# Optimization experiments

Measured on AMD Instinct MI355X. Metric: run time of the kernel, lower is better.

## Reference

```python
import jax, jax.numpy as jnp
import numpy as np

N_NODES = 1_000_000   # G.number_of_nodes()
F = 128               # feature_size
ED = 32               # embedding_dim = 2**int(log2(F/4))
N_CAT = 1000          # int64 feature cardinality
DF = 32               # float32 feature dim
L = [524288, 131072, 32768, 8192]  # nodeflow layer sizes (0..n_layers)
FAN = 10              # sampling fanout per block
N_LAYERS = 3


def lrelu(x, slope=0.1):
    return jnp.where(x >= 0, x, slope * x)


def setup_inputs() -> dict:
    key = jax.random.key(0)
    ks = iter(jax.random.split(key, 64))
    inp = {}
    # --- nodeflow data per layer ---
    for i, Li in enumerate(L):
        inp[f"nid{i}"] = jax.random.randint(next(ks), (Li,), 0, N_NODES)
        inp[f"cat{i}"] = jax.random.randint(next(ks), (Li,), 0, N_CAT)
        inp[f"feat{i}"] = jax.random.normal(next(ks), (Li, DF), jnp.float32)
    # --- block edge lists (src in layer b, dst in layer b+1, fanout FAN) ---
    for b in range(N_LAYERS):
        E = L[b + 1] * FAN
        inp[f"src{b}"] = jax.random.randint(next(ks), (E,), 0, L[b])
        inp[f"dst{b}"] = jnp.repeat(jnp.arange(L[b + 1]), FAN)
    # --- parameters ---
    def xav(shape):
        fan_in, fan_out = shape[0], shape[-1]
        s = float(np.sqrt(6.0 / (fan_in + fan_out)))
        return jax.random.uniform(next(ks), shape, jnp.float32, -s, s)
    inp["node_emb"] = jax.random.normal(next(ks), (N_NODES + 1, ED), jnp.float32) * (1.0 / ED)
    inp["exp_W"] = xav((ED, F)); inp["exp_b"] = jax.random.normal(next(ks), (F,), jnp.float32) * 0.001
    emb_cat = jax.random.normal(next(ks), (N_CAT, F), jnp.float32) * (1.0 / F)
    inp["emb_cat"] = emb_cat.at[0].set(0.0)  # padding_idx=0
    inp["proj_W"] = xav((DF, F)); inp["proj_b"] = jax.random.normal(next(ks), (F,), jnp.float32) * 0.001
    inp["d_W1"] = xav((F, F)); inp["d_b1"] = jax.random.normal(next(ks), (F,), jnp.float32) * 0.001
    inp["d_W2"] = xav((F, F)); inp["d_b2"] = jax.random.normal(next(ks), (F,), jnp.float32) * 0.001
    # GraphSAGE convs: depth-2 MLP on [h, mean_agg] per block (stacked over blocks)
    inp["conv_W1"] = jnp.stack([xav((2 * F, F)) for _ in range(N_LAYERS)])
    inp["conv_b1"] = jax.random.normal(next(ks), (N_LAYERS, F), jnp.float32) * 0.001
    inp["conv_W2"] = jnp.stack([xav((F, F)) for _ in range(N_LAYERS)])
    inp["conv_b2"] = jax.random.normal(next(ks), (N_LAYERS, F), jnp.float32) * 0.001
    return inp


def reference(nid0, nid1, nid2, nid3, cat0, cat1, cat2, cat3,
              feat0, feat1, feat2, feat3,
              src0, src1, src2, dst0, dst1, dst2,
              node_emb, exp_W, exp_b, emb_cat, proj_W, proj_b,
              d_W1, d_b1, d_W2, d_b2, conv_W1, conv_b1, conv_W2, conv_b2):
    nids = [nid0, nid1, nid2, nid3]
    cats = [cat0, cat1, cat2, cat3]
    feats = [feat0, feat1, feat2, feat3]
    srcs = [src0, src1, src2]
    dsts = [dst0, dst1, dst2]

    # per-layer node init: h = expansion(node_emb[nid+1]); then mix external features
    hs = []
    for i in range(N_LAYERS + 1):
        h = lrelu(node_emb[nids[i] + 1] @ exp_W + exp_b, 0.1)          # [Li, F]
        extra = emb_cat[cats[i]] + lrelu(feats[i] @ proj_W + proj_b, 0.01)
        mix = lrelu(lrelu(extra @ d_W1 + d_b1, 0.1) @ d_W2 + d_b2, 0.1)
        hs.append(h + mix)

    # block_compute: copy_src('h') + sum -> h_agg, copy_src('one') + sum -> w
    for b in range(N_LAYERS):
        n_dst = hs[b + 1].shape[0]
        msg = hs[b][srcs[b]]                                            # [E, F] gather
        h_agg = jax.ops.segment_sum(msg, dsts[b], num_segments=n_dst)
        w = jax.ops.segment_sum(jnp.ones(msg.shape[0], msg.dtype), dsts[b], num_segments=n_dst)
        mean = h_agg / jnp.maximum(w, 1.0)[:, None]
        hc = jnp.concatenate([hs[b + 1], mean], axis=-1)                # [n_dst, 2F]
        hn = lrelu(hc @ conv_W1[b] + conv_b1[b], 0.1)
        hn = hn @ conv_W2[b] + conv_b2[b]
        if b == N_LAYERS - 1:  # prediction layer: L2-normalize
            hn = hn / jnp.maximum(jnp.linalg.norm(hn, axis=1, keepdims=True), 1e-6)
        else:
            hn = lrelu(hn, 0.1)
        hs[b + 1] = hn
    return hs[N_LAYERS]
```

## Files before the change

### kernel.cpp

```cpp
#include <hip/hip_runtime.h>


typedef __attribute__((ext_vector_type(8))) short short8;
typedef __attribute__((ext_vector_type(4))) float f32x4;

__device__ __forceinline__ float lrelu(float x, float s) { return x >= 0.0f ? x : s * x; }

__device__ __forceinline__ unsigned short f2bf(float x) {
    unsigned u = __float_as_uint(x);
    unsigned r = (u + 0x7FFFu + ((u >> 16) & 1u)) >> 16;
    return (unsigned short)r;
}
__device__ __forceinline__ float bf2f(unsigned short u) {
    return __uint_as_float(((unsigned)u) << 16);
}

#define W_EXP   0
#define W_PROJ  4096
#define W_D1    8192
#define W_D2    24576
#define W_C1    40960
#define W_C2    139264
#define W_TOTAL 188416

__global__ __launch_bounds__(256)
void prep_weights(const float* __restrict__ expW, const float* __restrict__ projW,
                  const float* __restrict__ dW1, const float* __restrict__ dW2,
                  const float* __restrict__ cW1, const float* __restrict__ cW2,
                  unsigned short* __restrict__ dst)
{
    int gid = blockIdx.x * 256 + threadIdx.x;
    if (gid >= W_TOTAL) return;
    const float* src; int e, dbase;
    if (gid < W_PROJ)      { src = expW;  e = gid;          dbase = W_EXP; }
    else if (gid < W_D1)   { src = projW; e = gid - W_PROJ; dbase = W_PROJ; }
    else if (gid < W_D2)   { src = dW1;   e = gid - W_D1;   dbase = W_D1; }
    else if (gid < W_C1)   { src = dW2;   e = gid - W_D2;   dbase = W_D2; }
    else if (gid < W_C2)   { int r = gid - W_C1; int b = r / 32768; int w = r % 32768;
                             src = cW1 + (size_t)b * 32768; e = w; dbase = W_C1 + b * 32768; }
    else                   { int r = gid - W_C2; int b = r / 16384; int w = r % 16384;
                             src = cW2 + (size_t)b * 16384; e = w; dbase = W_C2 + b * 16384; }
    int k = e >> 7, f = e & 127;
    int kc = k >> 5, kr = k & 31, ft = f >> 4;
    int lane = ((kr >> 3) << 4) | (f & 15);
    int j = kr & 7;
    dst[dbase + ((kc * 8 + ft) * 64 + lane) * 8 + j] = f2bf(src[e]);
}

__global__ __launch_bounds__(256, 4)
void init_layer(const int* __restrict__ nid, const int* __restrict__ cat,
                const float* __restrict__ feat,
                const float* __restrict__ node_emb,
                const unsigned short* __restrict__ wExp, const float* __restrict__ exp_b,
                const float* __restrict__ emb_cat,
                const unsigned short* __restrict__ wProj, const float* __restrict__ proj_b,
                const unsigned short* __restrict__ wD1, const float* __restrict__ db1,
                const unsigned short* __restrict__ wD2, const float* __restrict__ db2,
                unsigned short* __restrict__ out)
{
    __shared__ __align__(16) unsigned short s_a[64][40];
    __shared__ __align__(16) unsigned short s_f[64][40];
    __shared__ __align__(16) unsigned short s_x[64][136];

    const int t = threadIdx.x;
    const int base = blockIdx.x * 64;

    {
        const int n = t >> 2, q = t & 3;
        const float* er = node_emb + ((size_t)(nid[base + n] + 1)) * 32 + q * 8;
        const float* fr = feat + ((size_t)(base + n)) * 32 + q * 8;
        short8 va, vf;
        #pragma unroll
        for (int i = 0; i < 8; ++i) { va[i] = (short)f2bf(er[i]); vf[i] = (short)f2bf(fr[i]); }
        *(short8*)&s_a[n][q * 8] = va;
        *(short8*)&s_f[n][q * 8] = vf;
    }
    __syncthreads();

    const int w = t >> 6, l = t & 63;
    const int lr = l & 15;
    const int lk = (l >> 4) * 8;
    const int rn0 = (l >> 4) * 4;

    short8 aE = *(const short8*)&s_a[w * 16 + lr][lk];
    short8 aF = *(const short8*)&s_f[w * 16 + lr][lk];
    f32x4 acch[8], accp[8];
    const f32x4 zero = {0.f, 0.f, 0.f, 0.f};
    #pragma unroll
    for (int ft = 0; ft < 8; ++ft) {
        short8 bE = *(const short8*)&wExp[(ft * 64 + l) * 8];
        short8 bP = *(const short8*)&wProj[(ft * 64 + l) * 8];
        acch[ft] = __builtin_amdgcn_mfma_f32_16x16x32_bf16(aE, bE, zero, 0, 0, 0);
        accp[ft] = __builtin_amdgcn_mfma_f32_16x16x32_bf16(aF, bP, zero, 0, 0, 0);
    }

    int cidx[4];
    #pragma unroll
    for (int r = 0; r < 4; ++r) cidx[r] = cat[base + w * 16 + rn0 + r];
    float pb[8], eb[8];
    #pragma unroll
    for (int ft = 0; ft < 8; ++ft) { pb[ft] = proj_b[ft * 16 + lr]; eb[ft] = exp_b[ft * 16 + lr]; }
    #pragma unroll
    for (int r = 0; r < 4; ++r) {
        const float* ecrow = emb_cat + (size_t)cidx[r] * 128;
        #pragma unroll
        for (int ft = 0; ft < 8; ++ft) {
            float ex = ecrow[ft * 16 + lr] + lrelu(accp[ft][r] + pb[ft], 0.01f);
            s_x[w * 16 + rn0 + r][ft * 16 + lr] = f2bf(ex);
            acch[ft][r] = lrelu(acch[ft][r] + eb[ft], 0.1f);
        }
    }
    __syncthreads();

    f32x4 acc[8];
    #pragma unroll
    for (int ft = 0; ft < 8; ++ft) acc[ft] = zero;
    #pragma unroll
    for (int kc = 0; kc < 4; ++kc) {
        short8 a = *(const short8*)&s_x[w * 16 + lr][kc * 32 + lk];
        #pragma unroll
        for (int ft = 0; ft < 8; ++ft) {
            short8 b = *(const short8*)&wD1[((kc * 8 + ft) * 64 + l) * 8];
            acc[ft] = __builtin_amdgcn_mfma_f32_16x16x32_bf16(a, b, acc[ft], 0, 0, 0);
        }
    }
    __syncthreads();
    #pragma unroll
    for (int ft = 0; ft < 8; ++ft)
        #pragma unroll
        for (int r = 0; r < 4; ++r)
            s_x[w * 16 + rn0 + r][ft * 16 + lr] = f2bf(lrelu(acc[ft][r] + db1[ft * 16 + lr], 0.1f));
    __syncthreads();

    #pragma unroll
    for (int ft = 0; ft < 8; ++ft) acc[ft] = zero;
    #pragma unroll
    for (int kc = 0; kc < 4; ++kc) {
        short8 a = *(const short8*)&s_x[w * 16 + lr][kc * 32 + lk];
        #pragma unroll
        for (int ft = 0; ft < 8; ++ft) {
            short8 b = *(const short8*)&wD2[((kc * 8 + ft) * 64 + l) * 8];
            acc[ft] = __builtin_amdgcn_mfma_f32_16x16x32_bf16(a, b, acc[ft], 0, 0, 0);
        }
    }
    __syncthreads();
    #pragma unroll
    for (int ft = 0; ft < 8; ++ft)
        #pragma unroll
        for (int r = 0; r < 4; ++r)
            s_x[w * 16 + rn0 + r][ft * 16 + lr] =
                f2bf(acch[ft][r] + lrelu(acc[ft][r] + db2[ft * 16 + lr], 0.1f));
    __syncthreads();

    {
        const int n = t >> 2, q = t & 3;
        short8* dstv = (short8*)(out + (size_t)(base + n) * 128 + q * 32);
        #pragma unroll
        for (int i = 0; i < 4; ++i) dstv[i] = *(const short8*)&s_x[n][q * 32 + i * 8];
    }
}

__global__ __launch_bounds__(256, 4)
void conv_layer(const unsigned short* __restrict__ h_src,
                unsigned short* __restrict__ h_self,
                float* __restrict__ out_f32,
                const int* __restrict__ src,
                const unsigned short* __restrict__ wC1, const float* __restrict__ b1,
                const unsigned short* __restrict__ wC2, const float* __restrict__ b2,
                int do_norm)
{
    __shared__ __align__(16) unsigned short s_x[64][264];
    float* xf = (float*)s_x;

    const int t = threadIdx.x;
    const int base = blockIdx.x * 64;
    const int n = t >> 2, q = t & 3;

    {
        const short8* selfp = (const short8*)(h_self + (size_t)(base + n) * 128 + q * 32);
        #pragma unroll
        for (int i = 0; i < 4; ++i) *(short8*)&s_x[n][q * 32 + i * 8] = selfp[i];

        float m[32];
        #pragma unroll
        for (int i = 0; i < 32; ++i) m[i] = 0.f;
        const int* sp = src + (size_t)(base + n) * 10;
        for (int e = 0; e < 10; ++e) {
            const short8* rp = (const short8*)(h_src + (size_t)sp[e] * 128 + q * 32);
            #pragma unroll
            for (int i = 0; i < 4; ++i) {
                short8 v = rp[i];
                #pragma unroll
                for (int j = 0; j < 8; ++j) m[i * 8 + j] += bf2f((unsigned short)v[j]);
            }
        }
        #pragma unroll
        for (int i = 0; i < 4; ++i) {
            short8 pm;
            #pragma unroll
            for (int j = 0; j < 8; ++j) pm[j] = (short)f2bf(m[i * 8 + j] * 0.1f);
            *(short8*)&s_x[n][128 + q * 32 + i * 8] = pm;
        }
    }
    __syncthreads();

    const int w = t >> 6, l = t & 63;
    const int lr = l & 15, lk = (l >> 4) * 8, rn0 = (l >> 4) * 4;
    const f32x4 zero = {0.f, 0.f, 0.f, 0.f};

    f32x4 acc[8];
    #pragma unroll
    for (int ft = 0; ft < 8; ++ft) acc[ft] = zero;
    #pragma unroll
    for (int kc = 0; kc < 8; ++kc) {
        short8 a = *(const short8*)&s_x[w * 16 + lr][kc * 32 + lk];
        #pragma unroll
        for (int ft = 0; ft < 8; ++ft) {
            short8 b = *(const short8*)&wC1[((kc * 8 + ft) * 64 + l) * 8];
            acc[ft] = __builtin_amdgcn_mfma_f32_16x16x32_bf16(a, b, acc[ft], 0, 0, 0);
        }
    }
    __syncthreads();
    #pragma unroll
    for (int ft = 0; ft < 8; ++ft)
        #pragma unroll
        for (int r = 0; r < 4; ++r)
            s_x[w * 16 + rn0 + r][ft * 16 + lr] = f2bf(lrelu(acc[ft][r] + b1[ft * 16 + lr], 0.1f));
    __syncthreads();

    f32x4 acc2[8];
    #pragma unroll
    for (int ft = 0; ft < 8; ++ft) acc2[ft] = zero;
    #pragma unroll
    for (int kc = 0; kc < 4; ++kc) {
        short8 a = *(const short8*)&s_x[w * 16 + lr][kc * 32 + lk];
        #pragma unroll
        for (int ft = 0; ft < 8; ++ft) {
            short8 b = *(const short8*)&wC2[((kc * 8 + ft) * 64 + l) * 8];
            acc2[ft] = __builtin_amdgcn_mfma_f32_16x16x32_bf16(a, b, acc2[ft], 0, 0, 0);
        }
    }
    __syncthreads();

    if (!do_norm) {
        #pragma unroll
        for (int ft = 0; ft < 8; ++ft)
            #pragma unroll
            for (int r = 0; r < 4; ++r)
                s_x[w * 16 + rn0 + r][ft * 16 + lr] =
                    f2bf(lrelu(acc2[ft][r] + b2[ft * 16 + lr], 0.1f));
        __syncthreads();
        short8* dstv = (short8*)(h_self + (size_t)(base + n) * 128 + q * 32);
        #pragma unroll
        for (int i = 0; i < 4; ++i) dstv[i] = *(const short8*)&s_x[n][q * 32 + i * 8];
    } else {
        #pragma unroll
        for (int ft = 0; ft < 8; ++ft)
            #pragma unroll
            for (int r = 0; r < 4; ++r)
                xf[(w * 16 + rn0 + r) * 132 + ft * 16 + lr] = acc2[ft][r] + b2[ft * 16 + lr];
        __syncthreads();
        f32x4 v[8];
        float ss = 0.f;
        #pragma unroll
        for (int c = 0; c < 8; ++c) {
            v[c] = *(const f32x4*)&xf[n * 132 + q * 32 + c * 4];
            ss += v[c][0] * v[c][0] + v[c][1] * v[c][1] + v[c][2] * v[c][2] + v[c][3] * v[c][3];
        }
        ss += __shfl_xor(ss, 1);
        ss += __shfl_xor(ss, 2);
        const float sc = 1.0f / fmaxf(sqrtf(ss), 1e-6f);
        float* op = out_f32 + (size_t)(base + n) * 128 + q * 32;
        #pragma unroll
        for (int c = 0; c < 8; ++c) {
            f32x4 o = {v[c][0] * sc, v[c][1] * sc, v[c][2] * sc, v[c][3] * sc};
            *(f32x4*)&op[c * 4] = o;
        }
    }
}

extern "C" void kernel_launch(void* const* d_in, const int* in_sizes, int n_in,
                              void* d_out, int out_size, void* d_ws, size_t ws_size,
                              hipStream_t stream)
{
    const int* nid[4]  = {(const int*)d_in[0], (const int*)d_in[3], (const int*)d_in[6], (const int*)d_in[9]};
    const int* cat[4]  = {(const int*)d_in[1], (const int*)d_in[4], (const int*)d_in[7], (const int*)d_in[10]};
    const float* feat[4] = {(const float*)d_in[2], (const float*)d_in[5], (const float*)d_in[8], (const float*)d_in[11]};
    const int* src[3]  = {(const int*)d_in[12], (const int*)d_in[14], (const int*)d_in[16]};
    const float* node_emb = (const float*)d_in[18];
    const float* exp_W  = (const float*)d_in[19];
    const float* exp_b  = (const float*)d_in[20];
    const float* emb_cat = (const float*)d_in[21];
    const float* proj_W = (const float*)d_in[22];
    const float* proj_b = (const float*)d_in[23];
    const float* dW1    = (const float*)d_in[24];
    const float* db1    = (const float*)d_in[25];
    const float* dW2    = (const float*)d_in[26];
    const float* db2    = (const float*)d_in[27];
    const float* cW1    = (const float*)d_in[28];
    const float* cb1    = (const float*)d_in[29];
    const float* cW2    = (const float*)d_in[30];
    const float* cb2    = (const float*)d_in[31];

    const int L[4] = {524288, 131072, 32768, 8192};
    unsigned short* hs[4];
    hs[0] = (unsigned short*)d_ws;
    hs[1] = hs[0] + (size_t)L[0] * 128;
    hs[2] = hs[1] + (size_t)L[1] * 128;
    hs[3] = hs[2] + (size_t)L[2] * 128;
    unsigned short* wfrag = hs[3] + (size_t)L[3] * 128;

    prep_weights<<<(W_TOTAL + 255) / 256, 256, 0, stream>>>(
        exp_W, proj_W, dW1, dW2, cW1, cW2, wfrag);

    for (int i = 0; i < 4; ++i) {
        init_layer<<<L[i] / 64, 256, 0, stream>>>(
            nid[i], cat[i], feat[i], node_emb,
            wfrag + W_EXP, exp_b, emb_cat,
            wfrag + W_PROJ, proj_b,
            wfrag + W_D1, db1, wfrag + W_D2, db2, hs[i]);
    }
    for (int b = 0; b < 3; ++b) {
        conv_layer<<<L[b + 1] / 64, 256, 0, stream>>>(
            hs[b], hs[b + 1], (b == 2) ? (float*)d_out : nullptr, src[b],
            wfrag + W_C1 + b * 32768, cb1 + (size_t)b * 128,
            wfrag + W_C2 + b * 16384, cb2 + (size_t)b * 128,
            (b == 2) ? 1 : 0);
    }
}
```

Baseline: 736.0 us.

## Merge init layers into one launch, use 512-thread blocks, bf16 emb_cat

Replaces the four per-layer init launches with a single init_all kernel that maps block index ranges to layers through a pointer struct. Both init and conv kernels now run 8 waves per 64-row tile, each wave computing half the output feature tiles, which halves per-wave accumulator registers and doubles threads per tile. The emb_cat table is pre-converted to bf16 in the weight prep kernel, the A operands are loaded straight into registers instead of staged through LDS, and the residual h is kept packed in bf16 registers. In exchange, weight fragments are loaded redundantly across waves and rounding on emb_cat and the residual changes slightly.

```diff
diff --git a/kernel.cpp b/kernel.cpp
--- a/kernel.cpp
+++ b/kernel.cpp
@@ -5,11 +5,9 @@
 typedef __attribute__((ext_vector_type(4))) float f32x4;
 
 __device__ __forceinline__ float lrelu(float x, float s) { return x >= 0.0f ? x : s * x; }
-
 __device__ __forceinline__ unsigned short f2bf(float x) {
     unsigned u = __float_as_uint(x);
-    unsigned r = (u + 0x7FFFu + ((u >> 16) & 1u)) >> 16;
-    return (unsigned short)r;
+    return (unsigned short)((u + 0x7FFFu + ((u >> 16) & 1u)) >> 16);
 }
 __device__ __forceinline__ float bf2f(unsigned short u) {
     return __uint_as_float(((unsigned)u) << 16);
@@ -21,25 +19,28 @@
 #define W_D2    24576
 #define W_C1    40960
 #define W_C2    139264
-#define W_TOTAL 188416
+#define W_EC    188416
+#define W_TOTAL 316416
 
 __global__ __launch_bounds__(256)
 void prep_weights(const float* __restrict__ expW, const float* __restrict__ projW,
                   const float* __restrict__ dW1, const float* __restrict__ dW2,
                   const float* __restrict__ cW1, const float* __restrict__ cW2,
+                  const float* __restrict__ embcat,
                   unsigned short* __restrict__ dst)
 {
     int gid = blockIdx.x * 256 + threadIdx.x;
     if (gid >= W_TOTAL) return;
+    if (gid >= W_EC) { int e = gid - W_EC; dst[W_EC + e] = f2bf(embcat[e]); return; }
     const float* src; int e, dbase;
     if (gid < W_PROJ)      { src = expW;  e = gid;          dbase = W_EXP; }
     else if (gid < W_D1)   { src = projW; e = gid - W_PROJ; dbase = W_PROJ; }
     else if (gid < W_D2)   { src = dW1;   e = gid - W_D1;   dbase = W_D1; }
     else if (gid < W_C1)   { src = dW2;   e = gid - W_D2;   dbase = W_D2; }
-    else if (gid < W_C2)   { int r = gid - W_C1; int b = r / 32768; int w = r % 32768;
-                             src = cW1 + (size_t)b * 32768; e = w; dbase = W_C1 + b * 32768; }
-    else                   { int r = gid - W_C2; int b = r / 16384; int w = r % 16384;
-                             src = cW2 + (size_t)b * 16384; e = w; dbase = W_C2 + b * 16384; }
+    else if (gid < W_C2)   { int r = gid - W_C1; int b = r / 32768; int w2 = r % 32768;
+                             src = cW1 + (size_t)b * 32768; e = w2; dbase = W_C1 + b * 32768; }
+    else                   { int r = gid - W_C2; int b = r / 16384; int w2 = r % 16384;
+                             src = cW2 + (size_t)b * 16384; e = w2; dbase = W_C2 + b * 16384; }
     int k = e >> 7, f = e & 127;
     int kc = k >> 5, kr = k & 31, ft = f >> 4;
     int lane = ((kr >> 3) << 4) | (f & 15);
@@ -47,120 +48,143 @@
     dst[dbase + ((kc * 8 + ft) * 64 + lane) * 8 + j] = f2bf(src[e]);
 }
 
-__global__ __launch_bounds__(256, 4)
-void init_layer(const int* __restrict__ nid, const int* __restrict__ cat,
-                const float* __restrict__ feat,
-                const float* __restrict__ node_emb,
-                const unsigned short* __restrict__ wExp, const float* __restrict__ exp_b,
-                const float* __restrict__ emb_cat,
-                const unsigned short* __restrict__ wProj, const float* __restrict__ proj_b,
-                const unsigned short* __restrict__ wD1, const float* __restrict__ db1,
-                const unsigned short* __restrict__ wD2, const float* __restrict__ db2,
-                unsigned short* __restrict__ out)
+struct GArgs {
+    const int* nid[4];
+    const int* cat[4];
+    const float* feat[4];
+    unsigned short* out[4];
+};
+
+__global__ __launch_bounds__(512, 6)
+void init_all(GArgs P, const float* __restrict__ node_emb,
+              const unsigned short* __restrict__ wExp, const float* __restrict__ exp_b,
+              const unsigned short* __restrict__ ecb,
+              const unsigned short* __restrict__ wProj, const float* __restrict__ proj_b,
+              const unsigned short* __restrict__ wD1, const float* __restrict__ db1,
+              const unsigned short* __restrict__ wD2, const float* __restrict__ db2)
 {
-    __shared__ __align__(16) unsigned short s_a[64][40];
-    __shared__ __align__(16) unsigned short s_f[64][40];
     __shared__ __align__(16) unsigned short s_x[64][136];
 
+    int bk = blockIdx.x, layer, lb;
+    if (bk < 8192)       { layer = 0; lb = bk; }
+    else if (bk < 10240) { layer = 1; lb = bk - 8192; }
+    else if (bk < 10752) { layer = 2; lb = bk - 10240; }
+    else                 { layer = 3; lb = bk - 10752; }
+    const int* __restrict__ nid = P.nid[layer];
+    const int* __restrict__ cat = P.cat[layer];
+    const float* __restrict__ feat = P.feat[layer];
+    unsigned short* __restrict__ out = P.out[layer];
+    const int base = lb * 64;
+
     const int t = threadIdx.x;
-    const int base = blockIdx.x * 64;
+    const int w = t >> 6, l = t & 63;
+    const int rt = w >> 1;
+    const int fh = (w & 1) * 4;
+    const int lr = l & 15, lk = (l >> 4) * 8, rn0 = (l >> 4) * 4;
+    const int nrow = rt * 16 + lr;
+    const f32x4 zero = {0.f, 0.f, 0.f, 0.f};
+
+    const float* er = node_emb + (size_t)(nid[base + nrow] + 1) * 32 + lk;
+    const float* fr = feat + (size_t)(base + nrow) * 32 + lk;
+    short8 aE, aF;
+    #pragma unroll
+    for (int i = 0; i < 8; ++i) { aE[i] = (short)f2bf(er[i]); aF[i] = (short)f2bf(fr[i]); }
+
+    f32x4 acch[4], accp[4];
+    #pragma unroll
+    for (int ftl = 0; ftl < 4; ++ftl) {
+        short8 bE = *(const short8*)&wExp[((fh + ftl) * 64 + l) * 8];
+        short8 bP = *(const short8*)&wProj[((fh + ftl) * 64 + l) * 8];
+        acch[ftl] = __builtin_amdgcn_mfma_f32_16x16x32_bf16(aE, bE, zero, 0, 0, 0);
+        accp[ftl] = __builtin_amdgcn_mfma_f32_16x16x32_bf16(aF, bP, zero, 0, 0, 0);
+    }
+
+    int cidx[4];
+    #pragma unroll
+    for (int r = 0; r < 4; ++r) cidx[r] = cat[base + rt * 16 + rn0 + r];
+
+    #pragma unroll
+    for (int ftl = 0; ftl < 4; ++ftl) {
+        const int col = (fh + ftl) * 16 + lr;
+        const float pb = proj_b[col];
+        #pragma unroll
+        for (int r = 0; r < 4; ++r) {
+            float ex = bf2f(ecb[(size_t)cidx[r] * 128 + col]) + lrelu(accp[ftl][r] + pb, 0.01f);
+            s_x[rt * 16 + rn0 + r][col] = f2bf(ex);
+        }
+    }
+    unsigned hp[8];
+    #pragma unroll
+    for (int ftl = 0; ftl < 4; ++ftl) {
+        const float eb = exp_b[(fh + ftl) * 16 + lr];
+        #pragma unroll
+        for (int rp = 0; rp < 2; ++rp) {
+            unsigned lo = f2bf(lrelu(acch[ftl][rp * 2 + 0] + eb, 0.1f));
+            unsigned hi = f2bf(lrelu(acch[ftl][rp * 2 + 1] + eb, 0.1f));
+            hp[ftl * 2 + rp] = lo | (hi << 16);
+        }
+    }
+    __syncthreads();
+
+    f32x4 acc[4];
+    #pragma unroll
+    for (int ftl = 0; ftl < 4; ++ftl) acc[ftl] = zero;
+    #pragma unroll
+    for (int kc = 0; kc < 4; ++kc) {
+        short8 a = *(const short8*)&s_x[rt * 16 + lr][kc * 32 + lk];
+        #pragma unroll
+        for (int ftl = 0; ftl < 4; ++ftl) {
+            short8 b = *(const short8*)&wD1[((kc * 8 + fh + ftl) * 64 + l) * 8];
+            acc[ftl] = __builtin_amdgcn_mfma_f32_16x16x32_bf16(a, b, acc[ftl], 0, 0, 0);
+        }
+    }
+    __syncthreads();
+    #pragma unroll
+    for (int ftl = 0; ftl < 4; ++ftl) {
+        const int col = (fh + ftl) * 16 + lr;
+        const float bb = db1[col];
+        #pragma unroll
+        for (int r = 0; r < 4; ++r)
+            s_x[rt * 16 + rn0 + r][col] = f2bf(lrelu(acc[ftl][r] + bb, 0.1f));
+    }
+    __syncthreads();
+
+    f32x4 acc2[4];
+    #pragma unroll
+    for (int ftl = 0; ftl < 4; ++ftl) acc2[ftl] = zero;
+    #pragma unroll
+    for (int kc = 0; kc < 4; ++kc) {
+        short8 a = *(const short8*)&s_x[rt * 16 + lr][kc * 32 + lk];
+        #pragma unroll
+        for (int ftl = 0; ftl < 4; ++ftl) {
+            short8 b = *(const short8*)&wD2[((kc * 8 + fh + ftl) * 64 + l) * 8];
+            acc2[ftl] = __builtin_amdgcn_mfma_f32_16x16x32_bf16(a, b, acc2[ftl], 0, 0, 0);
+        }
+    }
+    __syncthreads();
+    #pragma unroll
+    for (int ftl = 0; ftl < 4; ++ftl) {
+        const int col = (fh + ftl) * 16 + lr;
+        const float bb = db2[col];
+        #pragma unroll
+        for (int rp = 0; rp < 2; ++rp) {
+            float h0 = bf2f((unsigned short)(hp[ftl * 2 + rp] & 0xffffu));
+            float h1 = bf2f((unsigned short)(hp[ftl * 2 + rp] >> 16));
+            s_x[rt * 16 + rn0 + rp * 2 + 0][col] = f2bf(h0 + lrelu(acc2[ftl][rp * 2 + 0] + bb, 0.1f));
+            s_x[rt * 16 + rn0 + rp * 2 + 1][col] = f2bf(h1 + lrelu(acc2[ftl][rp * 2 + 1] + bb, 0.1f));
+        }
+    }
+    __syncthreads();
 
     {
-        const int n = t >> 2, q = t & 3;
-        const float* er = node_emb + ((size_t)(nid[base + n] + 1)) * 32 + q * 8;
-        const float* fr = feat + ((size_t)(base + n)) * 32 + q * 8;
-        short8 va, vf;
-        #pragma unroll
-        for (int i = 0; i < 8; ++i) { va[i] = (short)f2bf(er[i]); vf[i] = (short)f2bf(fr[i]); }
-        *(short8*)&s_a[n][q * 8] = va;
-        *(short8*)&s_f[n][q * 8] = vf;
-    }
-    __syncthreads();
-
-    const int w = t >> 6, l = t & 63;
-    const int lr = l & 15;
-    const int lk = (l >> 4) * 8;
-    const int rn0 = (l >> 4) * 4;
-
-    short8 aE = *(const short8*)&s_a[w * 16 + lr][lk];
-    short8 aF = *(const short8*)&s_f[w * 16 + lr][lk];
-    f32x4 acch[8], accp[8];
-    const f32x4 zero = {0.f, 0.f, 0.f, 0.f};
-    #pragma unroll
-    for (int ft = 0; ft < 8; ++ft) {
-        short8 bE = *(const short8*)&wExp[(ft * 64 + l) * 8];
-        short8 bP = *(const short8*)&wProj[(ft * 64 + l) * 8];
-        acch[ft] = __builtin_amdgcn_mfma_f32_16x16x32_bf16(aE, bE, zero, 0, 0, 0);
-        accp[ft] = __builtin_amdgcn_mfma_f32_16x16x32_bf16(aF, bP, zero, 0, 0, 0);
-    }
-
-    int cidx[4];
-    #pragma unroll
-    for (int r = 0; r < 4; ++r) cidx[r] = cat[base + w * 16 + rn0 + r];
-    float pb[8], eb[8];
-    #pragma unroll
-    for (int ft = 0; ft < 8; ++ft) { pb[ft] = proj_b[ft * 16 + lr]; eb[ft] = exp_b[ft * 16 + lr]; }
-    #pragma unroll
-    for (int r = 0; r < 4; ++r) {
-        const float* ecrow = emb_cat + (size_t)cidx[r] * 128;
-        #pragma unroll
-        for (int ft = 0; ft < 8; ++ft) {
-            float ex = ecrow[ft * 16 + lr] + lrelu(accp[ft][r] + pb[ft], 0.01f);
-            s_x[w * 16 + rn0 + r][ft * 16 + lr] = f2bf(ex);
-            acch[ft][r] = lrelu(acch[ft][r] + eb[ft], 0.1f);
-        }
-    }
-    __syncthreads();
-
-    f32x4 acc[8];
-    #pragma unroll
-    for (int ft = 0; ft < 8; ++ft) acc[ft] = zero;
-    #pragma unroll
-    for (int kc = 0; kc < 4; ++kc) {
-        short8 a = *(const short8*)&s_x[w * 16 + lr][kc * 32 + lk];
-        #pragma unroll
-        for (int ft = 0; ft < 8; ++ft) {
-            short8 b = *(const short8*)&wD1[((kc * 8 + ft) * 64 + l) * 8];
-            acc[ft] = __builtin_amdgcn_mfma_f32_16x16x32_bf16(a, b, acc[ft], 0, 0, 0);
-        }
-    }
-    __syncthreads();
-    #pragma unroll
-    for (int ft = 0; ft < 8; ++ft)
-        #pragma unroll
-        for (int r = 0; r < 4; ++r)
-            s_x[w * 16 + rn0 + r][ft * 16 + lr] = f2bf(lrelu(acc[ft][r] + db1[ft * 16 + lr], 0.1f));
-    __syncthreads();
-
-    #pragma unroll
-    for (int ft = 0; ft < 8; ++ft) acc[ft] = zero;
-    #pragma unroll
-    for (int kc = 0; kc < 4; ++kc) {
-        short8 a = *(const short8*)&s_x[w * 16 + lr][kc * 32 + lk];
-        #pragma unroll
-        for (int ft = 0; ft < 8; ++ft) {
-            short8 b = *(const short8*)&wD2[((kc * 8 + ft) * 64 + l) * 8];
-            acc[ft] = __builtin_amdgcn_mfma_f32_16x16x32_bf16(a, b, acc[ft], 0, 0, 0);
-        }
-    }
-    __syncthreads();
-    #pragma unroll
-    for (int ft = 0; ft < 8; ++ft)
-        #pragma unroll
-        for (int r = 0; r < 4; ++r)
-            s_x[w * 16 + rn0 + r][ft * 16 + lr] =
-                f2bf(acch[ft][r] + lrelu(acc[ft][r] + db2[ft * 16 + lr], 0.1f));
-    __syncthreads();
-
-    {
-        const int n = t >> 2, q = t & 3;
-        short8* dstv = (short8*)(out + (size_t)(base + n) * 128 + q * 32);
-        #pragma unroll
-        for (int i = 0; i < 4; ++i) dstv[i] = *(const short8*)&s_x[n][q * 32 + i * 8];
-    }
-}
-
-__global__ __launch_bounds__(256, 4)
+        const int n = t >> 3, q2 = t & 7;
+        short8* dstv = (short8*)(out + (size_t)(base + n) * 128 + q2 * 16);
+        dstv[0] = *(const short8*)&s_x[n][q2 * 16];
+        dstv[1] = *(const short8*)&s_x[n][q2 * 16 + 8];
+    }
+}
+
+__global__ __launch_bounds__(512, 6)
 void conv_layer(const unsigned short* __restrict__ h_src,
                 unsigned short* __restrict__ h_self,
                 float* __restrict__ out_f32,
@@ -174,105 +198,124 @@
 
     const int t = threadIdx.x;
     const int base = blockIdx.x * 64;
-    const int n = t >> 2, q = t & 3;
 
     {
-        const short8* selfp = (const short8*)(h_self + (size_t)(base + n) * 128 + q * 32);
-        #pragma unroll
-        for (int i = 0; i < 4; ++i) *(short8*)&s_x[n][q * 32 + i * 8] = selfp[i];
-
-        float m[32];
-        #pragma unroll
-        for (int i = 0; i < 32; ++i) m[i] = 0.f;
+        const int n = t >> 3, q2 = t & 7;
+        const int d0 = q2 * 16;
+        const short8* selfp = (const short8*)(h_self + (size_t)(base + n) * 128 + d0);
+        short8 s0 = selfp[0], s1 = selfp[1];
+        *(short8*)&s_x[n][d0] = s0;
+        *(short8*)&s_x[n][d0 + 8] = s1;
+
+        int si[10];
         const int* sp = src + (size_t)(base + n) * 10;
+        #pragma unroll
+        for (int e = 0; e < 10; ++e) si[e] = sp[e];
+        float m[16];
+        #pragma unroll
+        for (int i = 0; i < 16; ++i) m[i] = 0.f;
+        #pragma unroll
         for (int e = 0; e < 10; ++e) {
-            const short8* rp = (const short8*)(h_src + (size_t)sp[e] * 128 + q * 32);
+            const short8* rp = (const short8*)(h_src + (size_t)si[e] * 128 + d0);
+            short8 v0 = rp[0], v1 = rp[1];
             #pragma unroll
-            for (int i = 0; i < 4; ++i) {
-                short8 v = rp[i];
-                #pragma unroll
-                for (int j = 0; j < 8; ++j) m[i * 8 + j] += bf2f((unsigned short)v[j]);
+            for (int j = 0; j < 8; ++j) {
+                m[j]     += bf2f((unsigned short)v0[j]);
+                m[8 + j] += bf2f((unsigned short)v1[j]);
             }
         }
-        #pragma unroll
-        for (int i = 0; i < 4; ++i) {
-            short8 pm;
-            #pragma unroll
-            for (int j = 0; j < 8; ++j) pm[j] = (short)f2bf(m[i * 8 + j] * 0.1f);
-            *(short8*)&s_x[n][128 + q * 32 + i * 8] = pm;
-        }
+        short8 p0, p1;
+        #pragma unroll
+        for (int j = 0; j < 8; ++j) {
+            p0[j] = (short)f2bf(m[j] * 0.1f);
+            p1[j] = (short)f2bf(m[8 + j] * 0.1f);
+        }
+        *(short8*)&s_x[n][128 + d0] = p0;
+        *(short8*)&s_x[n][128 + d0 + 8] = p1;
     }
     __syncthreads();
 
     const int w = t >> 6, l = t & 63;
+    const int rt = w >> 1, fh = (w & 1) * 4;
     const int lr = l & 15, lk = (l >> 4) * 8, rn0 = (l >> 4) * 4;
     const f32x4 zero = {0.f, 0.f, 0.f, 0.f};
 
-    f32x4 acc[8];
-    #pragma unroll
-    for (int ft = 0; ft < 8; ++ft) acc[ft] = zero;
+    f32x4 acc[4];
+    #pragma unroll
+    for (int ftl = 0; ftl < 4; ++ftl) acc[ftl] = zero;
     #pragma unroll
     for (int kc = 0; kc < 8; ++kc) {
-        short8 a = *(const short8*)&s_x[w * 16 + lr][kc * 32 + lk];
-        #pragma unroll
-        for (int ft = 0; ft < 8; ++ft) {
-            short8 b = *(const short8*)&wC1[((kc * 8 + ft) * 64 + l) * 8];
-            acc[ft] = __builtin_amdgcn_mfma_f32_16x16x32_bf16(a, b, acc[ft], 0, 0, 0);
-        }
-    }
-    __syncthreads();
-    #pragma unroll
-    for (int ft = 0; ft < 8; ++ft)
+        short8 a = *(const short8*)&s_x[rt * 16 + lr][kc * 32 + lk];
+        #pragma unroll
+        for (int ftl = 0; ftl < 4; ++ftl) {
+            short8 b = *(const short8*)&wC1[((kc * 8 + fh + ftl) * 64 + l) * 8];
+            acc[ftl] = __builtin_amdgcn_mfma_f32_16x16x32_bf16(a, b, acc[ftl], 0, 0, 0);
+        }
+    }
+    __syncthreads();
+    #pragma unroll
+    for (int ftl = 0; ftl < 4; ++ftl) {
+        const int col = (fh + ftl) * 16 + lr;
+        const float bb = b1[col];
         #pragma unroll
         for (int r = 0; r < 4; ++r)
-            s_x[w * 16 + rn0 + r][ft * 16 + lr] = f2bf(lrelu(acc[ft][r] + b1[ft * 16 + lr], 0.1f));
-    __syncthreads();
-
-    f32x4 acc2[8];
-    #pragma unroll
-    for (int ft = 0; ft < 8; ++ft) acc2[ft] = zero;
+            s_x[rt * 16 + rn0 + r][col] = f2bf(lrelu(acc[ftl][r] + bb, 0.1f));
+    }
+    __syncthreads();
+
+    f32x4 acc2[4];
+    #pragma unroll
+    for (int ftl = 0; ftl < 4; ++ftl) acc2[ftl] = zero;
     #pragma unroll
     for (int kc = 0; kc < 4; ++kc) {
-        short8 a = *(const short8*)&s_x[w * 16 + lr][kc * 32 + lk];
-        #pragma unroll
-        for (int ft = 0; ft < 8; ++ft) {
-            short8 b = *(const short8*)&wC2[((kc * 8 + ft) * 64 + l) * 8];
-            acc2[ft] = __builtin_amdgcn_mfma_f32_16x16x32_bf16(a, b, acc2[ft], 0, 0, 0);
+        short8 a = *(const short8*)&s_x[rt * 16 + lr][kc * 32 + lk];
+        #pragma unroll
+        for (int ftl = 0; ftl < 4; ++ftl) {
+            short8 b = *(const short8*)&wC2[((kc * 8 + fh + ftl) * 64 + l) * 8];
+            acc2[ftl] = __builtin_amdgcn_mfma_f32_16x16x32_bf16(a, b, acc2[ftl], 0, 0, 0);
         }
     }
     __syncthreads();
 
     if (!do_norm) {
         #pragma unroll
-        for (int ft = 0; ft < 8; ++ft)
+        for (int ftl = 0; ftl < 4; ++ftl) {
+            const int col = (fh + ftl) * 16 + lr;
+            const float bb = b2[col];
             #pragma unroll
             for (int r = 0; r < 4; ++r)
-                s_x[w * 16 + rn0 + r][ft * 16 + lr] =
-                    f2bf(lrelu(acc2[ft][r] + b2[ft * 16 + lr], 0.1f));
+                s_x[rt * 16 + rn0 + r][col] = f2bf(lrelu(acc2[ftl][r] + bb, 0.1f));
+        }
         __syncthreads();
-        short8* dstv = (short8*)(h_self + (size_t)(base + n) * 128 + q * 32);
-        #pragma unroll
-        for (int i = 0; i < 4; ++i) dstv[i] = *(const short8*)&s_x[n][q * 32 + i * 8];
+        const int n = t >> 3, q2 = t & 7;
+        short8* dstv = (short8*)(h_self + (size_t)(base + n) * 128 + q2 * 16);
+        dstv[0] = *(const short8*)&s_x[n][q2 * 16];
+        dstv[1] = *(const short8*)&s_x[n][q2 * 16 + 8];
     } else {
         #pragma unroll
-        for (int ft = 0; ft < 8; ++ft)
+        for (int ftl = 0; ftl < 4; ++ftl) {
+            const int col = (fh + ftl) * 16 + lr;
+            const float bb = b2[col];
             #pragma unroll
             for (int r = 0; r < 4; ++r)
-                xf[(w * 16 + rn0 + r) * 132 + ft * 16 + lr] = acc2[ft][r] + b2[ft * 16 + lr];
+                xf[(rt * 16 + rn0 + r) * 132 + col] = acc2[ftl][r] + bb;
+        }
         __syncthreads();
-        f32x4 v[8];
+        const int n = t >> 3, q2 = t & 7;
+        f32x4 v[4];
         float ss = 0.f;
         #pragma unroll
-        for (int c = 0; c < 8; ++c) {
-            v[c] = *(const f32x4*)&xf[n * 132 + q * 32 + c * 4];
+        for (int c = 0; c < 4; ++c) {
+            v[c] = *(const f32x4*)&xf[n * 132 + q2 * 16 + c * 4];
             ss += v[c][0] * v[c][0] + v[c][1] * v[c][1] + v[c][2] * v[c][2] + v[c][3] * v[c][3];
         }
         ss += __shfl_xor(ss, 1);
         ss += __shfl_xor(ss, 2);
+        ss += __shfl_xor(ss, 4);
         const float sc = 1.0f / fmaxf(sqrtf(ss), 1e-6f);
-        float* op = out_f32 + (size_t)(base + n) * 128 + q * 32;
-        #pragma unroll
-        for (int c = 0; c < 8; ++c) {
+        float* op = out_f32 + (size_t)(base + n) * 128 + q2 * 16;
+        #pragma unroll
+        for (int c = 0; c < 4; ++c) {
             f32x4 o = {v[c][0] * sc, v[c][1] * sc, v[c][2] * sc, v[c][3] * sc};
             *(f32x4*)&op[c * 4] = o;
         }
@@ -283,10 +326,6 @@
                               void* d_out, int out_size, void* d_ws, size_t ws_size,
                               hipStream_t stream)
 {
-    const int* nid[4]  = {(const int*)d_in[0], (const int*)d_in[3], (const int*)d_in[6], (const int*)d_in[9]};
-    const int* cat[4]  = {(const int*)d_in[1], (const int*)d_in[4], (const int*)d_in[7], (const int*)d_in[10]};
-    const float* feat[4] = {(const float*)d_in[2], (const float*)d_in[5], (const float*)d_in[8], (const float*)d_in[11]};
-    const int* src[3]  = {(const int*)d_in[12], (const int*)d_in[14], (const int*)d_in[16]};
     const float* node_emb = (const float*)d_in[18];
     const float* exp_W  = (const float*)d_in[19];
     const float* exp_b  = (const float*)d_in[20];
@@ -308,23 +347,30 @@
     hs[1] = hs[0] + (size_t)L[0] * 128;
     hs[2] = hs[1] + (size_t)L[1] * 128;
     hs[3] = hs[2] + (size_t)L[2] * 128;
-    unsigned short* wfrag = hs[3] + (size_t)L[3] * 128;
+    unsigned short* wf = hs[3] + (size_t)L[3] * 128;
 
     prep_weights<<<(W_TOTAL + 255) / 256, 256, 0, stream>>>(
-        exp_W, proj_W, dW1, dW2, cW1, cW2, wfrag);
-
-    for (int i = 0; i < 4; ++i) {
-        init_layer<<<L[i] / 64, 256, 0, stream>>>(
-            nid[i], cat[i], feat[i], node_emb,
-            wfrag + W_EXP, exp_b, emb_cat,
-            wfrag + W_PROJ, proj_b,
-            wfrag + W_D1, db1, wfrag + W_D2, db2, hs[i]);
-    }
+        exp_W, proj_W, dW1, dW2, cW1, cW2, emb_cat, wf);
+
+    GArgs P;
+    P.nid[0] = (const int*)d_in[0]; P.nid[1] = (const int*)d_in[3];
+    P.nid[2] = (const int*)d_in[6]; P.nid[3] = (const int*)d_in[9];
+    P.cat[0] = (const int*)d_in[1]; P.cat[1] = (const int*)d_in[4];
+    P.cat[2] = (const int*)d_in[7]; P.cat[3] = (const int*)d_in[10];
+    P.feat[0] = (const float*)d_in[2]; P.feat[1] = (const float*)d_in[5];
+    P.feat[2] = (const float*)d_in[8]; P.feat[3] = (const float*)d_in[11];
+    P.out[0] = hs[0]; P.out[1] = hs[1]; P.out[2] = hs[2]; P.out[3] = hs[3];
+
+    init_all<<<10880, 512, 0, stream>>>(
+        P, node_emb, wf + W_EXP, exp_b, wf + W_EC,
+        wf + W_PROJ, proj_b, wf + W_D1, db1, wf + W_D2, db2);
+
+    const int* src[3] = {(const int*)d_in[12], (const int*)d_in[14], (const int*)d_in[16]};
     for (int b = 0; b < 3; ++b) {
-        conv_layer<<<L[b + 1] / 64, 256, 0, stream>>>(
+        conv_layer<<<L[b + 1] / 64, 512, 0, stream>>>(
             hs[b], hs[b + 1], (b == 2) ? (float*)d_out : nullptr, src[b],
-            wfrag + W_C1 + b * 32768, cb1 + (size_t)b * 128,
-            wfrag + W_C2 + b * 16384, cb2 + (size_t)b * 128,
+            wf + W_C1 + b * 32768, cb1 + (size_t)b * 128,
+            wf + W_C2 + b * 16384, cb2 + (size_t)b * 128,
             (b == 2) ? 1 : 0);
     }
 }
```

Measured after the change: 630.8 us. 14.3% less time.
